# Performance work log

Measured on AMD Instinct MI355X. Metric: run time of the kernel, lower is better.

Reference implementation:

```python
import jax, jax.numpy as jnp
import numpy as np
from jax import lax

B, S, H, K = 4, 4096, 2048, 4

def setup_inputs() -> dict:
    key = jax.random.key(0)
    k1, k2 = jax.random.split(key)
    hidden_states = jax.random.normal(k1, (B, S, H), dtype=jnp.float32)
    weight = jax.random.normal(k2, (H, K), dtype=jnp.float32)  # depthwise conv weight [H, k]
    attention_mask_2d = jnp.ones((B, S), dtype=jnp.float32)
    return {"hidden_states": hidden_states, "weight": weight, "attention_mask_2d": attention_mask_2d}

def reference(hidden_states, weight, attention_mask_2d):
    # Causal depthwise conv1d: left-pad k-1, groups == channels.
    h = hidden_states.shape[-1]
    k = weight.shape[-1]
    x = jnp.transpose(hidden_states, (0, 2, 1))  # [B, H, S]
    y = lax.conv_general_dilated(
        x,
        weight[:, None, :],          # [H, 1, k] (O, I/groups, W)
        window_strides=(1,),
        padding=[(k - 1, 0)],        # causal left pad
        feature_group_count=h,
        dimension_numbers=("NCH", "OIH", "NCH"),
    )
    y = jnp.transpose(y, (0, 2, 1))  # [B, S, H]
    return y * attention_mask_2d[:, :, None]
```

## Files before the change

kernel.cpp:

```cpp
#include <hip/hip_runtime.h>
#include <stdint.h>


constexpr int B_    = 4;
constexpr int S_    = 4096;
constexpr int H_    = 2048;
constexpr int H4    = H_ / 4;
constexpr int TPB   = 512;
constexpr int TROWS = 4;
constexpr int TILE4 = TROWS * H4;
constexpr int SPANR = 32;
constexpr int NT    = SPANR / TROWS;
constexpr int NBLK  = B_ * S_ / SPANR;

typedef float f32x4 __attribute__((ext_vector_type(4)));

__device__ __forceinline__ void stage_tile(const float4* gsrc, float4* lbuf,
                                           int wv, int ln) {
    #pragma unroll
    for (int j = 0; j < 4; ++j) {
        const int fo = (wv * 4 + j) * 64;
        __builtin_amdgcn_global_load_lds(
            (const __attribute__((address_space(1))) void*)(gsrc + fo + ln),
            (__attribute__((address_space(3))) void*)(lbuf + fo),
            16, 0, 0);
    }
}

__device__ __forceinline__ f32x4 conv_row(const float4& x3, const float4& x2,
                                          const float4& x1, const float4& x0,
                                          const float4& w0, const float4& w1,
                                          const float4& w2, const float4& w3,
                                          float m) {
    f32x4 o;
    o.x = fmaf(x3.x, w0.x, fmaf(x2.x, w0.y, fmaf(x1.x, w0.z, x0.x * w0.w)));
    o.y = fmaf(x3.y, w1.x, fmaf(x2.y, w1.y, fmaf(x1.y, w1.z, x0.y * w1.w)));
    o.z = fmaf(x3.z, w2.x, fmaf(x2.z, w2.y, fmaf(x1.z, w2.z, x0.z * w2.w)));
    o.w = fmaf(x3.w, w3.x, fmaf(x2.w, w3.y, fmaf(x1.w, w3.z, x0.w * w3.w)));
    o.x *= m; o.y *= m; o.z *= m; o.w *= m;
    return o;
}

__global__ __launch_bounds__(TPB, 4) void budgie_dwconv1d_kernel(
    const float* __restrict__ x,
    const float* __restrict__ w,
    const float* __restrict__ mask,
    float* __restrict__ y)
{
    __shared__ float4 buf[2][TILE4];

    const int t  = threadIdx.x;
    const int wv = t >> 6;
    const int ln = t & 63;
    const int r0 = blockIdx.x * SPANR;

    const float4* x4 = (const float4*)x;
    const float4* w4 = (const float4*)w;
    f32x4* y4 = (f32x4*)y;

    const float4 w0 = w4[t * 4 + 0];
    const float4 w1 = w4[t * 4 + 1];
    const float4 w2 = w4[t * 4 + 2];
    const float4 w3 = w4[t * 4 + 3];

    const float4 zero4 = make_float4(0.f, 0.f, 0.f, 0.f);

    float4 h1, h2, h3;
    if (r0 >= 3) {
        h1 = x4[(long)(r0 - 1) * H4 + t];
        h2 = x4[(long)(r0 - 2) * H4 + t];
        h3 = x4[(long)(r0 - 3) * H4 + t];
    } else {
        h1 = h2 = h3 = zero4;
    }

    stage_tile(x4 + (long)r0 * H4, buf[0], wv, ln);
    asm volatile("s_waitcnt vmcnt(0)" ::: "memory");
    __builtin_amdgcn_sched_barrier(0);
    __builtin_amdgcn_s_barrier();

    for (int i = 0; i < NT; ++i) {
        const int R = r0 + i * TROWS;
        const int p = i & 1;

        if (i + 1 < NT) {
            stage_tile(x4 + (long)(R + TROWS) * H4, buf[1 - p], wv, ln);
            asm volatile("s_waitcnt vmcnt(8)" ::: "memory");
        } else {
            asm volatile("s_waitcnt vmcnt(4)" ::: "memory");
        }
        __builtin_amdgcn_sched_barrier(0);
        __builtin_amdgcn_s_barrier();

        const float4 L0 = buf[p][0 * H4 + t];
        const float4 L1 = buf[p][1 * H4 + t];
        const float4 L2 = buf[p][2 * H4 + t];
        const float4 L3 = buf[p][3 * H4 + t];

        if ((R & (S_ - 1)) == 0) { h1 = h2 = h3 = zero4; }

        const int Ru = __builtin_amdgcn_readfirstlane(R);

        f32x4 o0 = conv_row(h3, h2, h1, L0, w0, w1, w2, w3, mask[Ru + 0]);
        f32x4 o1 = conv_row(h2, h1, L0, L1, w0, w1, w2, w3, mask[Ru + 1]);
        f32x4 o2 = conv_row(h1, L0, L1, L2, w0, w1, w2, w3, mask[Ru + 2]);
        f32x4 o3 = conv_row(L0, L1, L2, L3, w0, w1, w2, w3, mask[Ru + 3]);

        __builtin_nontemporal_store(o0, y4 + (long)(R + 0) * H4 + t);
        __builtin_nontemporal_store(o1, y4 + (long)(R + 1) * H4 + t);
        __builtin_nontemporal_store(o2, y4 + (long)(R + 2) * H4 + t);
        __builtin_nontemporal_store(o3, y4 + (long)(R + 3) * H4 + t);

        h1 = L3; h2 = L2; h3 = L1;

        __builtin_amdgcn_s_barrier();
    }
}

extern "C" void kernel_launch(void* const* d_in, const int* in_sizes, int n_in,
                              void* d_out, int out_size, void* d_ws, size_t ws_size,
                              hipStream_t stream) {
    const float* x    = (const float*)d_in[0];
    const float* w    = (const float*)d_in[1];
    const float* mask = (const float*)d_in[2];
    float* y = (float*)d_out;

    budgie_dwconv1d_kernel<<<dim3(NBLK), TPB, 0, stream>>>(x, w, mask, y);
}
```

Baseline: 239.1 us.

## Replace double-buffered 4-row tiles with single-buffer 16-row epochs

Restructures the kernel from a double-buffered pipeline of 4-row tiles into a single 16-row LDS buffer processed in four epochs per block. All 16 outputs are computed into registers, the next 16-row tile is staged into the same buffer, and then the stores are issued. The aim is fewer barriers and larger batches of loads in flight per block. In exchange it drops the overlap between loading and compute within a block, full vmcnt(0) waits serialize the load phase, and register and LDS use rise, so occupancy is halved via launch_bounds.

Result: slower. 246.3 us, median of 2 (+3.0%).

```diff
diff --git a/kernel.cpp b/kernel.cpp
--- a/kernel.cpp
+++ b/kernel.cpp
@@ -1,5 +1,4 @@
 #include <hip/hip_runtime.h>
-#include <stdint.h>
 
 
 constexpr int B_    = 4;
@@ -7,19 +6,19 @@
 constexpr int H_    = 2048;
 constexpr int H4    = H_ / 4;
 constexpr int TPB   = 512;
-constexpr int TROWS = 4;
-constexpr int TILE4 = TROWS * H4;
-constexpr int SPANR = 32;
-constexpr int NT    = SPANR / TROWS;
-constexpr int NBLK  = B_ * S_ / SPANR;
+constexpr int EROWS = 16;
+constexpr int NEP   = 4;
+constexpr int SPANR = EROWS * NEP;
+constexpr int NBLK  = (B_ * S_) / SPANR;
+constexpr int LDS4  = EROWS * H4;
 
 typedef float f32x4 __attribute__((ext_vector_type(4)));
 
-__device__ __forceinline__ void stage_tile(const float4* gsrc, float4* lbuf,
-                                           int wv, int ln) {
+__device__ __forceinline__ void stage16(const float4* gsrc, float4* lbuf,
+                                        int wv, int ln) {
     #pragma unroll
-    for (int j = 0; j < 4; ++j) {
-        const int fo = (wv * 4 + j) * 64;
+    for (int j = 0; j < 16; ++j) {
+        const int fo = (wv * 16 + j) * 64;
         __builtin_amdgcn_global_load_lds(
             (const __attribute__((address_space(1))) void*)(gsrc + fo + ln),
             (__attribute__((address_space(3))) void*)(lbuf + fo),
@@ -27,27 +26,13 @@
     }
 }
 
-__device__ __forceinline__ f32x4 conv_row(const float4& x3, const float4& x2,
-                                          const float4& x1, const float4& x0,
-                                          const float4& w0, const float4& w1,
-                                          const float4& w2, const float4& w3,
-                                          float m) {
-    f32x4 o;
-    o.x = fmaf(x3.x, w0.x, fmaf(x2.x, w0.y, fmaf(x1.x, w0.z, x0.x * w0.w)));
-    o.y = fmaf(x3.y, w1.x, fmaf(x2.y, w1.y, fmaf(x1.y, w1.z, x0.y * w1.w)));
-    o.z = fmaf(x3.z, w2.x, fmaf(x2.z, w2.y, fmaf(x1.z, w2.z, x0.z * w2.w)));
-    o.w = fmaf(x3.w, w3.x, fmaf(x2.w, w3.y, fmaf(x1.w, w3.z, x0.w * w3.w)));
-    o.x *= m; o.y *= m; o.z *= m; o.w *= m;
-    return o;
-}
-
-__global__ __launch_bounds__(TPB, 4) void budgie_dwconv1d_kernel(
+__global__ __launch_bounds__(TPB, 2) void budgie_dwconv1d_kernel(
     const float* __restrict__ x,
     const float* __restrict__ w,
     const float* __restrict__ mask,
     float* __restrict__ y)
 {
-    __shared__ float4 buf[2][TILE4];
+    __shared__ float4 lbuf[LDS4];
 
     const int t  = threadIdx.x;
     const int wv = t >> 6;
@@ -65,55 +50,50 @@
 
     const float4 zero4 = make_float4(0.f, 0.f, 0.f, 0.f);
 
-    float4 h1, h2, h3;
-    if (r0 >= 3) {
-        h1 = x4[(long)(r0 - 1) * H4 + t];
-        h2 = x4[(long)(r0 - 2) * H4 + t];
-        h3 = x4[(long)(r0 - 3) * H4 + t];
+    float4 wm3, wm2, wm1;
+    if ((r0 & (S_ - 1)) != 0) {
+        wm1 = x4[(long)(r0 - 1) * H4 + t];
+        wm2 = x4[(long)(r0 - 2) * H4 + t];
+        wm3 = x4[(long)(r0 - 3) * H4 + t];
     } else {
-        h1 = h2 = h3 = zero4;
+        wm1 = wm2 = wm3 = zero4;
     }
 
-    stage_tile(x4 + (long)r0 * H4, buf[0], wv, ln);
+    stage16(x4 + (long)r0 * H4, lbuf, wv, ln);
     asm volatile("s_waitcnt vmcnt(0)" ::: "memory");
     __builtin_amdgcn_sched_barrier(0);
-    __builtin_amdgcn_s_barrier();
 
-    for (int i = 0; i < NT; ++i) {
-        const int R = r0 + i * TROWS;
-        const int p = i & 1;
+    #pragma unroll
+    for (int e = 0; e < NEP; ++e) {
+        const int R  = r0 + e * EROWS;
+        const int Ru = __builtin_amdgcn_readfirstlane(R);
 
-        if (i + 1 < NT) {
-            stage_tile(x4 + (long)(R + TROWS) * H4, buf[1 - p], wv, ln);
-            asm volatile("s_waitcnt vmcnt(8)" ::: "memory");
-        } else {
-            asm volatile("s_waitcnt vmcnt(4)" ::: "memory");
+        __builtin_amdgcn_s_barrier();
+        f32x4 o[EROWS];
+        #pragma unroll
+        for (int r = 0; r < EROWS; ++r) {
+            const float4 cur = lbuf[r * H4 + t];
+            const float  m   = mask[Ru + r];
+            o[r].x = fmaf(wm3.x, w0.x, fmaf(wm2.x, w0.y, fmaf(wm1.x, w0.z, cur.x * w0.w)));
+            o[r].y = fmaf(wm3.y, w1.x, fmaf(wm2.y, w1.y, fmaf(wm1.y, w1.z, cur.y * w1.w)));
+            o[r].z = fmaf(wm3.z, w2.x, fmaf(wm2.z, w2.y, fmaf(wm1.z, w2.z, cur.z * w2.w)));
+            o[r].w = fmaf(wm3.w, w3.x, fmaf(wm2.w, w3.y, fmaf(wm1.w, w3.z, cur.w * w3.w)));
+            o[r].x *= m; o[r].y *= m; o[r].z *= m; o[r].w *= m;
+            wm3 = wm2; wm2 = wm1; wm1 = cur;
         }
-        __builtin_amdgcn_sched_barrier(0);
         __builtin_amdgcn_s_barrier();
 
-        const float4 L0 = buf[p][0 * H4 + t];
-        const float4 L1 = buf[p][1 * H4 + t];
-        const float4 L2 = buf[p][2 * H4 + t];
-        const float4 L3 = buf[p][3 * H4 + t];
+        asm volatile("s_waitcnt vmcnt(0)" ::: "memory");
+        __builtin_amdgcn_sched_barrier(0);
 
-        if ((R & (S_ - 1)) == 0) { h1 = h2 = h3 = zero4; }
+        if (e + 1 < NEP)
+            stage16(x4 + (long)(R + EROWS) * H4, lbuf, wv, ln);
+        asm volatile("s_waitcnt vmcnt(0)" ::: "memory");
+        __builtin_amdgcn_sched_barrier(0);
 
-        const int Ru = __builtin_amdgcn_readfirstlane(R);
-
-        f32x4 o0 = conv_row(h3, h2, h1, L0, w0, w1, w2, w3, mask[Ru + 0]);
-        f32x4 o1 = conv_row(h2, h1, L0, L1, w0, w1, w2, w3, mask[Ru + 1]);
-        f32x4 o2 = conv_row(h1, L0, L1, L2, w0, w1, w2, w3, mask[Ru + 2]);
-        f32x4 o3 = conv_row(L0, L1, L2, L3, w0, w1, w2, w3, mask[Ru + 3]);
-
-        __builtin_nontemporal_store(o0, y4 + (long)(R + 0) * H4 + t);
-        __builtin_nontemporal_store(o1, y4 + (long)(R + 1) * H4 + t);
-        __builtin_nontemporal_store(o2, y4 + (long)(R + 2) * H4 + t);
-        __builtin_nontemporal_store(o3, y4 + (long)(R + 3) * H4 + t);
-
-        h1 = L3; h2 = L2; h3 = L1;
-
-        __builtin_amdgcn_s_barrier();
+        #pragma unroll
+        for (int r = 0; r < EROWS; ++r)
+            __builtin_nontemporal_store(o[r], y4 + (long)(R + r) * H4 + t);
     }
 }
 
```

## Replace double-buffered 4-row tiles with a 4-deep ring of 2-row tiles

Applied to the files above, without the earlier changes.

Splits each staged tile into 2 rows and keeps a 4-slot LDS ring, so three tiles are in flight ahead of the compute instead of one. The loop is fully unrolled, and the vmcnt waits are set per iteration to cover the ramp-up and drain phases. Memory latency should be better hidden while LDS use stays the same. It also drops the per-iteration batch-boundary reset by loading the halo only when the block does not start a sequence. The hand-counted vmcnt values are fragile: they depend on the stores also counting toward vmcnt, and there are twice as many barriers per row.

After: 237.1 us. Within noise of the previous version (-0.8%).

```diff
diff --git a/kernel.cpp b/kernel.cpp
--- a/kernel.cpp
+++ b/kernel.cpp
@@ -1,5 +1,4 @@
 #include <hip/hip_runtime.h>
-#include <stdint.h>
 
 
 constexpr int B_    = 4;
@@ -7,7 +6,7 @@
 constexpr int H_    = 2048;
 constexpr int H4    = H_ / 4;
 constexpr int TPB   = 512;
-constexpr int TROWS = 4;
+constexpr int TROWS = 2;
 constexpr int TILE4 = TROWS * H4;
 constexpr int SPANR = 32;
 constexpr int NT    = SPANR / TROWS;
@@ -15,11 +14,11 @@
 
 typedef float f32x4 __attribute__((ext_vector_type(4)));
 
-__device__ __forceinline__ void stage_tile(const float4* gsrc, float4* lbuf,
-                                           int wv, int ln) {
+__device__ __forceinline__ void stage2(const float4* gsrc, float4* lbuf,
+                                       int wv, int ln) {
     #pragma unroll
-    for (int j = 0; j < 4; ++j) {
-        const int fo = (wv * 4 + j) * 64;
+    for (int j = 0; j < 2; ++j) {
+        const int fo = (wv * 2 + j) * 64;
         __builtin_amdgcn_global_load_lds(
             (const __attribute__((address_space(1))) void*)(gsrc + fo + ln),
             (__attribute__((address_space(3))) void*)(lbuf + fo),
@@ -47,7 +46,7 @@
     const float* __restrict__ mask,
     float* __restrict__ y)
 {
-    __shared__ float4 buf[2][TILE4];
+    __shared__ float4 ring[4][TILE4];
 
     const int t  = threadIdx.x;
     const int wv = t >> 6;
@@ -66,7 +65,7 @@
     const float4 zero4 = make_float4(0.f, 0.f, 0.f, 0.f);
 
     float4 h1, h2, h3;
-    if (r0 >= 3) {
+    if ((r0 & (S_ - 1)) != 0) {
         h1 = x4[(long)(r0 - 1) * H4 + t];
         h2 = x4[(long)(r0 - 2) * H4 + t];
         h3 = x4[(long)(r0 - 3) * H4 + t];
@@ -74,44 +73,39 @@
         h1 = h2 = h3 = zero4;
     }
 
-    stage_tile(x4 + (long)r0 * H4, buf[0], wv, ln);
-    asm volatile("s_waitcnt vmcnt(0)" ::: "memory");
-    __builtin_amdgcn_sched_barrier(0);
-    __builtin_amdgcn_s_barrier();
+    stage2(x4 + (long)(r0 + 0 * TROWS) * H4, ring[0], wv, ln);
+    stage2(x4 + (long)(r0 + 1 * TROWS) * H4, ring[1], wv, ln);
+    stage2(x4 + (long)(r0 + 2 * TROWS) * H4, ring[2], wv, ln);
 
+    #pragma unroll
     for (int i = 0; i < NT; ++i) {
-        const int R = r0 + i * TROWS;
-        const int p = i & 1;
+        if (i + 3 < NT)
+            stage2(x4 + (long)(r0 + (i + 3) * TROWS) * H4, ring[(i + 3) & 3],
+                   wv, ln);
 
-        if (i + 1 < NT) {
-            stage_tile(x4 + (long)(R + TROWS) * H4, buf[1 - p], wv, ln);
+        if (i == 0 || i == NT - 1)
+            asm volatile("s_waitcnt vmcnt(6)" ::: "memory");
+        else if (i == 1 || i == NT - 2)
             asm volatile("s_waitcnt vmcnt(8)" ::: "memory");
-        } else {
-            asm volatile("s_waitcnt vmcnt(4)" ::: "memory");
-        }
+        else if (i == 2 || i == NT - 3)
+            asm volatile("s_waitcnt vmcnt(10)" ::: "memory");
+        else
+            asm volatile("s_waitcnt vmcnt(12)" ::: "memory");
         __builtin_amdgcn_sched_barrier(0);
         __builtin_amdgcn_s_barrier();
 
-        const float4 L0 = buf[p][0 * H4 + t];
-        const float4 L1 = buf[p][1 * H4 + t];
-        const float4 L2 = buf[p][2 * H4 + t];
-        const float4 L3 = buf[p][3 * H4 + t];
-
-        if ((R & (S_ - 1)) == 0) { h1 = h2 = h3 = zero4; }
-
+        const int R  = r0 + i * TROWS;
         const int Ru = __builtin_amdgcn_readfirstlane(R);
+        const float4 L0 = ring[i & 3][0 * H4 + t];
+        const float4 L1 = ring[i & 3][1 * H4 + t];
 
         f32x4 o0 = conv_row(h3, h2, h1, L0, w0, w1, w2, w3, mask[Ru + 0]);
         f32x4 o1 = conv_row(h2, h1, L0, L1, w0, w1, w2, w3, mask[Ru + 1]);
-        f32x4 o2 = conv_row(h1, L0, L1, L2, w0, w1, w2, w3, mask[Ru + 2]);
-        f32x4 o3 = conv_row(L0, L1, L2, L3, w0, w1, w2, w3, mask[Ru + 3]);
 
         __builtin_nontemporal_store(o0, y4 + (long)(R + 0) * H4 + t);
         __builtin_nontemporal_store(o1, y4 + (long)(R + 1) * H4 + t);
-        __builtin_nontemporal_store(o2, y4 + (long)(R + 2) * H4 + t);
-        __builtin_nontemporal_store(o3, y4 + (long)(R + 3) * H4 + t);
 
-        h1 = L3; h2 = L2; h3 = L1;
+        h3 = h1; h2 = L0; h1 = L1;
 
         __builtin_amdgcn_s_barrier();
     }
```
